# Kernel optimization log

Measured on AMD Instinct MI355X. Metric: run time of the kernel, lower is better.

Reference implementation:

```python
import jax, jax.numpy as jnp
import numpy as np

B, L, D = 16384, 5, 1024  # batch, lesionNum, feat_dim == att_dim
LN_EPS = 1e-5


def _layernorm(x, g, b):
    mu = jnp.mean(x, axis=-1, keepdims=True)
    var = jnp.var(x, axis=-1, keepdims=True)
    return (x - mu) * jax.lax.rsqrt(var + LN_EPS) * g + b


def setup_inputs() -> dict:
    key = jax.random.key(0)
    ks = jax.random.split(key, 8)
    s = 0.02
    x = jax.random.normal(ks[0], (B, L, D), dtype=jnp.float32)
    mask = jax.random.randint(ks[1], (1, L), 0, 2, dtype=jnp.int64)
    mask = mask.at[0, 0].set(1)  # guarantee at least one unmasked position
    Wq = jax.random.normal(ks[2], (D, D), dtype=jnp.float32) * s
    Wk = jax.random.normal(ks[3], (D, D), dtype=jnp.float32) * s
    Wv = jax.random.normal(ks[4], (D, D), dtype=jnp.float32) * s
    W1 = jax.random.normal(ks[5], (D, D), dtype=jnp.float32) * s
    b1 = jnp.zeros((D,), dtype=jnp.float32)
    W2 = jax.random.normal(ks[6], (D, D), dtype=jnp.float32) * s
    b2 = jnp.zeros((D,), dtype=jnp.float32)
    att_g = jnp.ones((D,), dtype=jnp.float32)
    att_b = jnp.zeros((D,), dtype=jnp.float32)
    ff_g = jnp.ones((D,), dtype=jnp.float32)
    ff_b = jnp.zeros((D,), dtype=jnp.float32)
    return dict(x=x, mask=mask, Wq=Wq, Wk=Wk, Wv=Wv, W1=W1, b1=b1, W2=W2,
                b2=b2, att_g=att_g, att_b=att_b, ff_g=ff_g, ff_b=ff_b)


def reference(x, mask, Wq, Wk, Wv, W1, b1, W2, b2, att_g, att_b, ff_g, ff_b):
    # QKV (no bias). With nhead=1 the reshape makes scores per-token dot
    # products: (B,L,1,D) @ (B,L,D,1) -> (B,L,1,1); we keep them as (B,L).
    q = jnp.einsum('bld,ed->ble', x, Wq)
    k = jnp.einsum('bld,ed->ble', x, Wk)
    v = jnp.einsum('bld,ed->ble', x, Wv)
    scores = jnp.sum(q * k, axis=-1) / jnp.sqrt(jnp.float32(D))  # (B,L)
    # torch loop sets -inf where ANY mask row has 0 (applied to all batches)
    keep = jnp.all(mask != 0, axis=0)  # (L,)
    scores = jnp.where(keep[None, :], scores, -jnp.inf)
    probs = jax.nn.softmax(scores, axis=1)  # softmax over token dim (dim=1)
    probs = jnp.where(jnp.isnan(probs), 0.0, probs)  # nan-safe (all-masked)
    attn = probs[:, :, None] * v  # (B,L,1,1)@(B,L,1,D) == per-token scaling
    y = _layernorm(attn + x, att_g, att_b)
    # FFN: Linear -> exact GELU -> Linear (dropout inactive in eval)
    h = jax.nn.gelu(jnp.einsum('bld,ed->ble', y, W1) + b1, approximate=False)
    ff = jnp.einsum('bld,ed->ble', h, W2) + b2
    return _layernorm(ff + y, ff_g, ff_b)
```

## Files before the change

### kernel.cpp

```cpp
#include <hip/hip_runtime.h>
#include <hip/hip_bf16.h>
#include <cstdint>


typedef float f32x4 __attribute__((ext_vector_type(4)));
typedef __bf16 bf16x8 __attribute__((ext_vector_type(8)));

#define DD 1024
#define NROWS 81920L

__device__ __forceinline__ unsigned short f2bf(float f) {
  union { float f; unsigned u; } c; c.f = f;
  unsigned u = c.u;
  return (unsigned short)((u + 0x7FFFu + ((u >> 16) & 1u)) >> 16);
}
__device__ __forceinline__ float bf2f(unsigned short b) {
  union { unsigned u; float f; } c; c.u = ((unsigned)b) << 16;
  return c.f;
}
__device__ __forceinline__ void unpack8(uint4 v, float* o) {
  o[0] = bf2f((unsigned short)(v.x & 0xffffu)); o[1] = bf2f((unsigned short)(v.x >> 16));
  o[2] = bf2f((unsigned short)(v.y & 0xffffu)); o[3] = bf2f((unsigned short)(v.y >> 16));
  o[4] = bf2f((unsigned short)(v.z & 0xffffu)); o[5] = bf2f((unsigned short)(v.z >> 16));
  o[6] = bf2f((unsigned short)(v.w & 0xffffu)); o[7] = bf2f((unsigned short)(v.w >> 16));
}
__device__ __forceinline__ void gload_lds16(const void* g, void* l) {
  __builtin_amdgcn_global_load_lds(
      (const __attribute__((address_space(1))) unsigned int*)g,
      (__attribute__((address_space(3))) unsigned int*)l, 16, 0, 0);
}

__global__ void __launch_bounds__(256) k_cvt_bf16(const float* __restrict__ in,
                                                  unsigned short* __restrict__ out, long n) {
  long i = ((long)blockIdx.x * blockDim.x + threadIdx.x) * 8;
  long stride = (long)gridDim.x * blockDim.x * 8;
  for (; i < n; i += stride) {
    f32x4 a = *(const f32x4*)(in + i);
    f32x4 b = *(const f32x4*)(in + i + 4);
    uint4 o;
    o.x = (unsigned)f2bf(a[0]) | ((unsigned)f2bf(a[1]) << 16);
    o.y = (unsigned)f2bf(a[2]) | ((unsigned)f2bf(a[3]) << 16);
    o.z = (unsigned)f2bf(b[0]) | ((unsigned)f2bf(b[1]) << 16);
    o.w = (unsigned)f2bf(b[2]) | ((unsigned)f2bf(b[3]) << 16);
    *(uint4*)(out + i) = o;
  }
}

__global__ void __launch_bounds__(256) k_gt(const float* __restrict__ Wq,
                                            const float* __restrict__ Wk,
                                            unsigned short* __restrict__ Gt) {
  __shared__ float sk[16][16];
  __shared__ float sq[16][64];
  const int tx = threadIdx.x, ty = threadIdx.y;
  const int n0 = blockIdx.y * 16;
  const int k0 = blockIdx.x * 64;
  float acc[4] = {0.f, 0.f, 0.f, 0.f};
  for (int e0 = 0; e0 < 1024; e0 += 16) {
    sk[ty][tx] = Wk[(long)(e0 + ty) * DD + n0 + tx];
    *(f32x4*)&sq[ty][tx * 4] = *(const f32x4*)&Wq[(long)(e0 + ty) * DD + k0 + tx * 4];
    __syncthreads();
#pragma unroll
    for (int ee = 0; ee < 16; ++ee) {
      float kv = sk[ee][ty];
      f32x4 qv = *(const f32x4*)&sq[ee][tx * 4];
      acc[0] += kv * qv[0]; acc[1] += kv * qv[1];
      acc[2] += kv * qv[2]; acc[3] += kv * qv[3];
    }
    __syncthreads();
  }
  uint2 o;
  o.x = (unsigned)f2bf(acc[0]) | ((unsigned)f2bf(acc[1]) << 16);
  o.y = (unsigned)f2bf(acc[2]) | ((unsigned)f2bf(acc[3]) << 16);
  *(uint2*)&Gt[(long)(n0 + ty) * DD + k0 + tx * 4] = o;
}


#define TILE(T, RSLOT, SSLOT, CA, CB, NA, NB, DOREAD, DOSTAGE, VM4)            \
  {                                                                            \
    if (VM4) { asm volatile("s_waitcnt vmcnt(4)" ::: "memory"); }              \
    else     { asm volatile("s_waitcnt vmcnt(0)" ::: "memory"); }              \
    __builtin_amdgcn_s_barrier();                                              \
    asm volatile("" ::: "memory");                                             \
    if (DOREAD) {                                                              \
      const char* bn_ = ldsB + (RSLOT) * 32768;                                \
      _Pragma("unroll") for (int mi = 0; mi < 8; ++mi)                         \
        NA[mi] = *(const bf16x8*)(bn_ + aoff[mi]);                             \
      _Pragma("unroll") for (int nj = 0; nj < 4; ++nj)                         \
        NB[nj] = *(const bf16x8*)(bn_ + 16384 + boff[nj]);                     \
    }                                                                          \
    if (DOSTAGE) stage((T) + 3, ldsB + (SSLOT) * 32768);                       \
    __builtin_amdgcn_sched_barrier(0);                                         \
    __builtin_amdgcn_s_setprio(1);                                             \
    _Pragma("unroll") for (int mi = 0; mi < 8; ++mi)                           \
      _Pragma("unroll") for (int nj = 0; nj < 4; ++nj)                         \
        acc[mi][nj] = __builtin_amdgcn_mfma_f32_16x16x32_bf16(                 \
            CA[mi], CB[nj], acc[mi][nj], 0, 0, 0);                             \
    __builtin_amdgcn_s_setprio(0);                                             \
  }

template <int EPI>
__global__ void __launch_bounds__(512, 2) k_gemm256(
    const unsigned short* __restrict__ A,
    const unsigned short* __restrict__ B,
    unsigned short* __restrict__ outb,
    float* __restrict__ outf,
    const float* __restrict__ bias,
    const unsigned short* __restrict__ resid,
    const int ntl2,
    const int cst) {
  __shared__ __align__(16) char ldsB[131072];
  const int tid = threadIdx.x;
  const int lane = tid & 63;
  const int wid = tid >> 6;
  const int wm = wid >> 2, wn = wid & 3;

  const int nwg = gridDim.x;
  const int cpx = nwg >> 3;
  const int dd = blockIdx.x;
  const int lgc = (dd & 7) * cpx + (dd >> 3);
  const int mt = lgc >> ntl2;
  const int nt = lgc & ((1 << ntl2) - 1);
  const long m0 = (long)mt * 256;
  const int n0 = nt * 256;

  const int srow = tid >> 2;
  const int oc = ((tid & 3) << 4) ^ (((srow >> 1) & 3) << 4);
  const char* gA0 = (const char*)A + (m0 + srow) * 2048 + oc;
  const char* gA1 = gA0 + 128 * 2048;
  const char* gB0 = (const char*)B + ((long)n0 + srow) * 2048 + oc;
  const char* gB1 = gB0 + 128 * 2048;
  const int d0 = tid * 16;

  auto stage = [&](int kt, char* base) {
    const long ko = (long)kt << 6;
    gload_lds16(gA0 + ko, base + d0);
    gload_lds16(gA1 + ko, base + 8192 + d0);
    gload_lds16(gB0 + ko, base + 16384 + d0);
    gload_lds16(gB1 + ko, base + 24576 + d0);
  };

  const int la = lane & 15, lg = lane >> 4;
  const int cb = ((lg ^ ((la >> 1) & 3)) << 4);
  int aoff[8], boff[4];
#pragma unroll
  for (int mi = 0; mi < 8; ++mi) aoff[mi] = (wm * 128 + mi * 16 + la) * 64 + cb;
#pragma unroll
  for (int nj = 0; nj < 4; ++nj) boff[nj] = (wn * 64 + nj * 16 + la) * 64 + cb;

  f32x4 acc[8][4];
#pragma unroll
  for (int mi = 0; mi < 8; ++mi)
#pragma unroll
    for (int nj = 0; nj < 4; ++nj) acc[mi][nj] = f32x4{0.f, 0.f, 0.f, 0.f};

  stage(0, ldsB);
  stage(1, ldsB + 32768);
  stage(2, ldsB + 65536);
  asm volatile("s_waitcnt vmcnt(8)" ::: "memory");
  __builtin_amdgcn_s_barrier();
  asm volatile("" ::: "memory");

  bf16x8 a0[8], b0[4], a1[8], b1[4];
#pragma unroll
  for (int mi = 0; mi < 8; ++mi) a0[mi] = *(const bf16x8*)(ldsB + aoff[mi]);
#pragma unroll
  for (int nj = 0; nj < 4; ++nj) b0[nj] = *(const bf16x8*)(ldsB + 16384 + boff[nj]);

  for (int t0 = 0; t0 < 28; t0 += 4) {
    TILE(t0 + 0, 1, 3, a0, b0, a1, b1, true, true, true);
    TILE(t0 + 1, 2, 0, a1, b1, a0, b0, true, true, true);
    TILE(t0 + 2, 3, 1, a0, b0, a1, b1, true, true, true);
    TILE(t0 + 3, 0, 2, a1, b1, a0, b0, true, true, true);
  }
  TILE(28, 1, 3, a0, b0, a1, b1, true, true, true);
  TILE(29, 2, 0, a1, b1, a0, b0, true, false, true);
  TILE(30, 3, 1, a0, b0, a1, b1, true, false, false);
  TILE(31, 0, 2, a1, b1, a0, b0, false, false, false);

  const long rbase = m0 + wm * 128 + (lane >> 4) * 4;
  const int cbase = n0 + wn * 64 + la;
#pragma unroll
  for (int mi = 0; mi < 8; ++mi) {
#pragma unroll
    for (int nj = 0; nj < 4; ++nj) {
      const int col = cbase + nj * 16;
      float bv = 0.f;
      if constexpr (EPI != 0) bv = bias[col];
#pragma unroll
      for (int t = 0; t < 4; ++t) {
        const long r = rbase + mi * 16 + t;
        float v = acc[mi][nj][t];
        if constexpr (EPI == 0) {
          outb[r * (long)cst + col] = f2bf(v);
        } else if constexpr (EPI == 1) {
          v += bv;
          v = 0.5f * v * (1.0f + erff(v * 0.70710678118654752f));
          outb[r * (long)cst + col] = f2bf(v);
        } else if constexpr (EPI == 2) {
          v += bv + bf2f(resid[r * (long)cst + col]);
          outf[r * (long)cst + col] = v;
        } else {
          v += bv + bf2f(resid[r * (long)cst + col]);
          outb[r * (long)cst + col] = f2bf(v);
        }
      }
    }
  }
}

__global__ void __launch_bounds__(256) k_attn_ln(
    const unsigned short* __restrict__ xb, const unsigned short* __restrict__ uv,
    unsigned short* __restrict__ yb, const int* __restrict__ mask,
    const float* __restrict__ att_g, const float* __restrict__ att_b) {
  const int b = blockIdx.x * 4 + (threadIdx.x >> 6);
  const int lane = threadIdx.x & 63;
  const long xbase = (long)b * 5120 + lane * 16;
  const long ubase = (long)b * 10240 + lane * 16;

  float xr[5][16];
  float sc[5];
#pragma unroll
  for (int l = 0; l < 5; ++l) {
    const unsigned short* xp = xb + xbase + l * 1024;
    const unsigned short* up = uv + ubase + l * 2048;
    unpack8(*(const uint4*)xp, xr[l]); unpack8(*(const uint4*)(xp + 8), xr[l] + 8);
    float uu[16];
    unpack8(*(const uint4*)up, uu); unpack8(*(const uint4*)(up + 8), uu + 8);
    float d = 0.f;
#pragma unroll
    for (int c = 0; c < 16; ++c) d += xr[l][c] * uu[c];
#pragma unroll
    for (int off = 32; off; off >>= 1) d += __shfl_xor(d, off);
    sc[l] = d * 0.03125f;
  }
  bool keep[5];
  float m = -1e30f;
#pragma unroll
  for (int l = 0; l < 5; ++l) {
    keep[l] = (mask[l] != 0);
    if (keep[l]) m = fmaxf(m, sc[l]);
  }
  float p[5], s = 0.f;
#pragma unroll
  for (int l = 0; l < 5; ++l) {
    p[l] = keep[l] ? __expf(sc[l] - m) : 0.f;
    s += p[l];
  }
  const float inv = 1.f / s;

  float gg[16], bb[16];
  {
    const float* gp = att_g + lane * 16;
    const float* bp = att_b + lane * 16;
#pragma unroll
    for (int q = 0; q < 4; ++q) {
      f32x4 gv = *(const f32x4*)(gp + q * 4);
      f32x4 bv = *(const f32x4*)(bp + q * 4);
#pragma unroll
      for (int c = 0; c < 4; ++c) { gg[q * 4 + c] = gv[c]; bb[q * 4 + c] = bv[c]; }
    }
  }

#pragma unroll
  for (int l = 0; l < 5; ++l) {
    const unsigned short* vp = uv + ubase + l * 2048 + 1024;
    float vv[16];
    unpack8(*(const uint4*)vp, vv); unpack8(*(const uint4*)(vp + 8), vv + 8);
    const float pl = p[l] * inv;
    float t[16], sm = 0.f, sq = 0.f;
#pragma unroll
    for (int c = 0; c < 16; ++c) {
      t[c] = pl * vv[c] + xr[l][c];
      sm += t[c];
      sq += t[c] * t[c];
    }
#pragma unroll
    for (int off = 32; off; off >>= 1) {
      sm += __shfl_xor(sm, off);
      sq += __shfl_xor(sq, off);
    }
    const float mu = sm * (1.f / 1024.f);
    const float var = sq * (1.f / 1024.f) - mu * mu;
    const float rs = rsqrtf(var + 1e-5f);
    unsigned short r[16];
#pragma unroll
    for (int c = 0; c < 16; ++c) r[c] = f2bf((t[c] - mu) * rs * gg[c] + bb[c]);
    uint4 o0, o1;
    o0.x = (unsigned)r[0] | ((unsigned)r[1] << 16);  o0.y = (unsigned)r[2] | ((unsigned)r[3] << 16);
    o0.z = (unsigned)r[4] | ((unsigned)r[5] << 16);  o0.w = (unsigned)r[6] | ((unsigned)r[7] << 16);
    o1.x = (unsigned)r[8] | ((unsigned)r[9] << 16);  o1.y = (unsigned)r[10] | ((unsigned)r[11] << 16);
    o1.z = (unsigned)r[12] | ((unsigned)r[13] << 16); o1.w = (unsigned)r[14] | ((unsigned)r[15] << 16);
    unsigned short* yp = yb + xbase + l * 1024;
    *(uint4*)yp = o0;
    *(uint4*)(yp + 8) = o1;
  }
}

__global__ void __launch_bounds__(256) k_ln_final_bf(const unsigned short* __restrict__ zb,
                                                     float* __restrict__ out,
                                                     const float* __restrict__ g,
                                                     const float* __restrict__ bb) {
  const int lane = threadIdx.x & 63;
  const long row = (long)blockIdx.x * 4 + (threadIdx.x >> 6);
  const unsigned short* p = zb + row * DD + lane * 16;
  float t[16];
  unpack8(*(const uint4*)p, t);
  unpack8(*(const uint4*)(p + 8), t + 8);
  float sm = 0.f, sq = 0.f;
#pragma unroll
  for (int c = 0; c < 16; ++c) { sm += t[c]; sq += t[c] * t[c]; }
#pragma unroll
  for (int off = 32; off; off >>= 1) {
    sm += __shfl_xor(sm, off);
    sq += __shfl_xor(sq, off);
  }
  const float mu = sm * (1.f / 1024.f);
  const float var = sq * (1.f / 1024.f) - mu * mu;
  const float rs = rsqrtf(var + 1e-5f);
  float* op = out + row * DD + lane * 16;
  const float* gp = g + lane * 16;
  const float* bp = bb + lane * 16;
#pragma unroll
  for (int q = 0; q < 4; ++q) {
    f32x4 gv = *(const f32x4*)(gp + q * 4);
    f32x4 bv = *(const f32x4*)(bp + q * 4);
    f32x4 o;
#pragma unroll
    for (int c = 0; c < 4; ++c) o[c] = (t[q * 4 + c] - mu) * rs * gv[c] + bv[c];
    *(f32x4*)(op + q * 4) = o;
  }
}

__global__ void __launch_bounds__(256) k_ln_final(float* __restrict__ z,
                                                  const float* __restrict__ g,
                                                  const float* __restrict__ bb) {
  const int lane = threadIdx.x & 63;
  const long row = (long)blockIdx.x * 4 + (threadIdx.x >> 6);
  float* p = z + row * DD + lane * 16;
  f32x4 v[4];
  float sm = 0.f, sq = 0.f;
#pragma unroll
  for (int q = 0; q < 4; ++q) {
    v[q] = *(const f32x4*)(p + q * 4);
#pragma unroll
    for (int c = 0; c < 4; ++c) { sm += v[q][c]; sq += v[q][c] * v[q][c]; }
  }
#pragma unroll
  for (int off = 32; off; off >>= 1) {
    sm += __shfl_xor(sm, off);
    sq += __shfl_xor(sq, off);
  }
  const float mu = sm * (1.f / 1024.f);
  const float var = sq * (1.f / 1024.f) - mu * mu;
  const float rs = rsqrtf(var + 1e-5f);
  const float* gp = g + lane * 16;
  const float* bp = bb + lane * 16;
#pragma unroll
  for (int q = 0; q < 4; ++q) {
    f32x4 gv = *(const f32x4*)(gp + q * 4);
    f32x4 bv = *(const f32x4*)(bp + q * 4);
#pragma unroll
    for (int c = 0; c < 4; ++c) v[q][c] = (v[q][c] - mu) * rs * gv[c] + bv[c];
    *(f32x4*)(p + q * 4) = v[q];
  }
}

extern "C" void kernel_launch(void* const* d_in, const int* in_sizes, int n_in,
                              void* d_out, int out_size, void* d_ws, size_t ws_size,
                              hipStream_t stream) {
  const float* x     = (const float*)d_in[0];
  const int*   mask  = (const int*)d_in[1];
  const float* Wq    = (const float*)d_in[2];
  const float* Wk    = (const float*)d_in[3];
  const float* Wv    = (const float*)d_in[4];
  const float* W1    = (const float*)d_in[5];
  const float* b1    = (const float*)d_in[6];
  const float* W2    = (const float*)d_in[7];
  const float* b2    = (const float*)d_in[8];
  const float* att_g = (const float*)d_in[9];
  const float* att_b = (const float*)d_in[10];
  const float* ff_g  = (const float*)d_in[11];
  const float* ff_b  = (const float*)d_in[12];

  const long NE = NROWS * DD;
  unsigned short* xb   = (unsigned short*)d_ws;
  unsigned short* hb   = xb + NE;
  unsigned short* Bcat = hb + NE;
  unsigned short* W1b  = Bcat + 2L * DD * DD;
  unsigned short* W2b  = W1b + (long)DD * DD;
  unsigned short* zb   = W2b + (long)DD * DD;

  const size_t need_zb = (size_t)(3L * NE + 4L * DD * DD) * 2;
  const bool use_zb = ws_size >= need_zb;

  unsigned short* uvb = (unsigned short*)d_out;
  float* outf = (float*)d_out;

  k_cvt_bf16<<<2048, 256, 0, stream>>>(x, xb, NE);
  k_cvt_bf16<<<512, 256, 0, stream>>>(Wv, Bcat + (long)DD * DD, (long)DD * DD);
  k_cvt_bf16<<<512, 256, 0, stream>>>(W1, W1b, (long)DD * DD);
  k_cvt_bf16<<<512, 256, 0, stream>>>(W2, W2b, (long)DD * DD);
  k_gt<<<dim3(16, 64), dim3(16, 16), 0, stream>>>(Wq, Wk, Bcat);

  k_gemm256<0><<<2560, 512, 0, stream>>>(xb, Bcat, uvb, nullptr, nullptr, nullptr, 3, 2048);
  k_attn_ln<<<4096, 256, 0, stream>>>(xb, uvb, xb, mask, att_g, att_b);
  k_gemm256<1><<<1280, 512, 0, stream>>>(xb, W1b, hb, nullptr, b1, nullptr, 2, 1024);
  if (use_zb) {
    k_gemm256<3><<<1280, 512, 0, stream>>>(hb, W2b, zb, nullptr, b2, xb, 2, 1024);
    k_ln_final_bf<<<20480, 256, 0, stream>>>(zb, outf, ff_g, ff_b);
  } else {
    k_gemm256<2><<<1280, 512, 0, stream>>>(hb, W2b, nullptr, outf, b2, xb, 2, 1024);
    k_ln_final<<<20480, 256, 0, stream>>>(outf, ff_g, ff_b);
  }
}
```

Measured before the change: 1.287 ms.

## Restructure GEMM main loop into 8-phase ping-pong schedule with split fragment loads

Replaces the 4-slot, register-double-buffered K loop with a two-buffer ping-pong over K=128 super-steps, each split into four phases. Every phase loads half of the A fragments plus the B fragments from LDS, issues one stage of the next super-step's A or B, and runs 16 MFMAs, with barriers between phases. The aim is lower register pressure, since only one fragment set is held instead of two, and finer interleaving of LDS reads, global-to-LDS copies and MFMA work. In exchange it adds more barriers per K step and waits on lgkmcnt(0) before each MFMA group, which exposes LDS read latency.

Result: faster. 1.247 ms (-3.1%).

```diff
diff --git a/kernel.cpp b/kernel.cpp
--- a/kernel.cpp
+++ b/kernel.cpp
@@ -75,27 +75,34 @@
 }
 
 
-#define TILE(T, RSLOT, SSLOT, CA, CB, NA, NB, DOREAD, DOSTAGE, VM4)            \
+#define PHASE(BUFC, KK, MIH, DOSTAGE, STG_ISB, STG_KK, SN, TRAILV)             \
   {                                                                            \
-    if (VM4) { asm volatile("s_waitcnt vmcnt(4)" ::: "memory"); }              \
-    else     { asm volatile("s_waitcnt vmcnt(0)" ::: "memory"); }              \
+    const char* rb_ = (BUFC) + ((KK) << 14);                                   \
+    if ((MIH) == 0) {                                                          \
+      _Pragma("unroll") for (int j = 0; j < 4; ++j)                            \
+        fb[j] = *(const bf16x8*)(rb_ + boff[j]);                               \
+      _Pragma("unroll") for (int i = 0; i < 4; ++i)                            \
+        fa[i] = *(const bf16x8*)(rb_ + aoff[i]);                               \
+    } else {                                                                   \
+      _Pragma("unroll") for (int i = 0; i < 4; ++i)                            \
+        fa[i] = *(const bf16x8*)(rb_ + aoff[4 + i]);                           \
+    }                                                                          \
+    if (DOSTAGE) {                                                             \
+      if (STG_ISB) stageB((SN), (STG_KK)); else stageA((SN), (STG_KK));        \
+    }                                                                          \
+    __builtin_amdgcn_s_barrier();                                              \
+    asm volatile("s_waitcnt lgkmcnt(0)" ::: "memory");                         \
+    __builtin_amdgcn_sched_barrier(0);                                         \
+    __builtin_amdgcn_s_setprio(1);                                             \
+    _Pragma("unroll") for (int i = 0; i < 4; ++i)                              \
+      _Pragma("unroll") for (int j = 0; j < 4; ++j)                            \
+        acc[(MIH) * 4 + i][j] = __builtin_amdgcn_mfma_f32_16x16x32_bf16(       \
+            fa[i], fb[j], acc[(MIH) * 4 + i][j], 0, 0, 0);                     \
+    __builtin_amdgcn_s_setprio(0);                                             \
+    if ((TRAILV) == 1) asm volatile("s_waitcnt vmcnt(4)" ::: "memory");        \
+    else if ((TRAILV) == 2) asm volatile("s_waitcnt vmcnt(0)" ::: "memory");   \
     __builtin_amdgcn_s_barrier();                                              \
     asm volatile("" ::: "memory");                                             \
-    if (DOREAD) {                                                              \
-      const char* bn_ = ldsB + (RSLOT) * 32768;                                \
-      _Pragma("unroll") for (int mi = 0; mi < 8; ++mi)                         \
-        NA[mi] = *(const bf16x8*)(bn_ + aoff[mi]);                             \
-      _Pragma("unroll") for (int nj = 0; nj < 4; ++nj)                         \
-        NB[nj] = *(const bf16x8*)(bn_ + 16384 + boff[nj]);                     \
-    }                                                                          \
-    if (DOSTAGE) stage((T) + 3, ldsB + (SSLOT) * 32768);                       \
-    __builtin_amdgcn_sched_barrier(0);                                         \
-    __builtin_amdgcn_s_setprio(1);                                             \
-    _Pragma("unroll") for (int mi = 0; mi < 8; ++mi)                           \
-      _Pragma("unroll") for (int nj = 0; nj < 4; ++nj)                         \
-        acc[mi][nj] = __builtin_amdgcn_mfma_f32_16x16x32_bf16(                 \
-            CA[mi], CB[nj], acc[mi][nj], 0, 0, 0);                             \
-    __builtin_amdgcn_s_setprio(0);                                             \
   }
 
 template <int EPI>
@@ -123,20 +130,23 @@
   const long m0 = (long)mt * 256;
   const int n0 = nt * 256;
 
-  const int srow = tid >> 2;
-  const int oc = ((tid & 3) << 4) ^ (((srow >> 1) & 3) << 4);
-  const char* gA0 = (const char*)A + (m0 + srow) * 2048 + oc;
-  const char* gA1 = gA0 + 128 * 2048;
-  const char* gB0 = (const char*)B + ((long)n0 + srow) * 2048 + oc;
-  const char* gB1 = gB0 + 128 * 2048;
-  const int d0 = tid * 16;
-
-  auto stage = [&](int kt, char* base) {
-    const long ko = (long)kt << 6;
-    gload_lds16(gA0 + ko, base + d0);
-    gload_lds16(gA1 + ko, base + 8192 + d0);
-    gload_lds16(gB0 + ko, base + 16384 + d0);
-    gload_lds16(gB1 + ko, base + 24576 + d0);
+  const int q = tid >> 2;
+  const int gcol = (((tid & 3) ^ ((q >> 1) & 3)) << 4);
+  const char* gA = (const char*)A + (m0 + q) * 2048 + gcol;
+  const char* gB = (const char*)B + ((long)n0 + q) * 2048 + gcol;
+  const int ldst = tid * 16;
+
+  auto stageA = [&](int s, int kk) {
+    char* dst = ldsB + ((s & 1) << 16) + (kk << 14) + ldst;
+    const char* src = gA + (long)s * 128 + (kk << 6);
+    gload_lds16(src, dst);
+    gload_lds16(src + 128 * 2048, dst + 8192);
+  };
+  auto stageB = [&](int s, int kk) {
+    char* dst = ldsB + ((s & 1) << 16) + 32768 + (kk << 14) + ldst;
+    const char* src = gB + (long)s * 128 + (kk << 6);
+    gload_lds16(src, dst);
+    gload_lds16(src + 128 * 2048, dst + 8192);
   };
 
   const int la = lane & 15, lg = lane >> 4;
@@ -145,7 +155,7 @@
 #pragma unroll
   for (int mi = 0; mi < 8; ++mi) aoff[mi] = (wm * 128 + mi * 16 + la) * 64 + cb;
 #pragma unroll
-  for (int nj = 0; nj < 4; ++nj) boff[nj] = (wn * 64 + nj * 16 + la) * 64 + cb;
+  for (int nj = 0; nj < 4; ++nj) boff[nj] = 32768 + (wn * 64 + nj * 16 + la) * 64 + cb;
 
   f32x4 acc[8][4];
 #pragma unroll
@@ -153,29 +163,28 @@
 #pragma unroll
     for (int nj = 0; nj < 4; ++nj) acc[mi][nj] = f32x4{0.f, 0.f, 0.f, 0.f};
 
-  stage(0, ldsB);
-  stage(1, ldsB + 32768);
-  stage(2, ldsB + 65536);
-  asm volatile("s_waitcnt vmcnt(8)" ::: "memory");
+  bf16x8 fa[4], fb[4];
+
+  stageA(0, 0); stageB(0, 0); stageA(0, 1); stageB(0, 1);
+  asm volatile("s_waitcnt vmcnt(4)" ::: "memory");
   __builtin_amdgcn_s_barrier();
   asm volatile("" ::: "memory");
 
-  bf16x8 a0[8], b0[4], a1[8], b1[4];
-#pragma unroll
-  for (int mi = 0; mi < 8; ++mi) a0[mi] = *(const bf16x8*)(ldsB + aoff[mi]);
-#pragma unroll
-  for (int nj = 0; nj < 4; ++nj) b0[nj] = *(const bf16x8*)(ldsB + 16384 + boff[nj]);
-
-  for (int t0 = 0; t0 < 28; t0 += 4) {
-    TILE(t0 + 0, 1, 3, a0, b0, a1, b1, true, true, true);
-    TILE(t0 + 1, 2, 0, a1, b1, a0, b0, true, true, true);
-    TILE(t0 + 2, 3, 1, a0, b0, a1, b1, true, true, true);
-    TILE(t0 + 3, 0, 2, a1, b1, a0, b0, true, true, true);
-  }
-  TILE(28, 1, 3, a0, b0, a1, b1, true, true, true);
-  TILE(29, 2, 0, a1, b1, a0, b0, true, false, true);
-  TILE(30, 3, 1, a0, b0, a1, b1, true, false, false);
-  TILE(31, 0, 2, a1, b1, a0, b0, false, false, false);
+  for (int s = 0; s < 15; ++s) {
+    const int sn = s + 1;
+    char* bufc = ldsB + ((s & 1) << 16);
+    PHASE(bufc, 0, 0, true, false, 0, sn, 0);
+    PHASE(bufc, 0, 1, true, true,  0, sn, 1);
+    PHASE(bufc, 1, 0, true, false, 1, sn, 0);
+    PHASE(bufc, 1, 1, true, true,  1, sn, 1);
+  }
+  {
+    char* bufc = ldsB + ((15 & 1) << 16);
+    PHASE(bufc, 0, 0, false, false, 0, 16, 0);
+    PHASE(bufc, 0, 1, false, false, 0, 16, 2);
+    PHASE(bufc, 1, 0, false, false, 1, 16, 0);
+    PHASE(bufc, 1, 1, false, false, 1, 16, 0);
+  }
 
   const long rbase = m0 + wm * 128 + (lane >> 4) * 4;
   const int cbase = n0 + wn * 64 + la;
```

## Fuse score dot-product into QKV GEMM epilogue and shorten LDS pipeline to three stages

Applied to the files above, without the earlier changes.

The first GEMM's epilogue now computes each row's partial score x·(G x) for its column tiles directly and writes 16 float partials per row. The u half of the output is no longer stored in bf16 and re-read; only v is written. The attention kernel then sums these partials instead of reloading u and computing dot products. Separately, the main GEMM loop changes from a 4-buffer prefetch-depth-3 schedule with register double-buffered fragments to a 3-buffer depth-2 schedule with the barrier after compute. This cuts LDS use, but LDS loads may now be less hidden.

New measurement: 1.271 ms. No clear change (-1.3%).

```diff
diff --git a/kernel.cpp b/kernel.cpp
--- a/kernel.cpp
+++ b/kernel.cpp
@@ -75,27 +75,28 @@
 }
 
 
-#define TILE(T, RSLOT, SSLOT, CA, CB, NA, NB, DOREAD, DOSTAGE, VM4)            \
+#define STEP(RBUF, SBUF, S, DOSTAGE, TAILV)                                    \
   {                                                                            \
-    if (VM4) { asm volatile("s_waitcnt vmcnt(4)" ::: "memory"); }              \
-    else     { asm volatile("s_waitcnt vmcnt(0)" ::: "memory"); }              \
-    __builtin_amdgcn_s_barrier();                                              \
-    asm volatile("" ::: "memory");                                             \
-    if (DOREAD) {                                                              \
-      const char* bn_ = ldsB + (RSLOT) * 32768;                                \
-      _Pragma("unroll") for (int mi = 0; mi < 8; ++mi)                         \
-        NA[mi] = *(const bf16x8*)(bn_ + aoff[mi]);                             \
-      _Pragma("unroll") for (int nj = 0; nj < 4; ++nj)                         \
-        NB[nj] = *(const bf16x8*)(bn_ + 16384 + boff[nj]);                     \
+    const char* bA_ = ldsB + (RBUF) * 32768;                                   \
+    const char* bB_ = bA_ + 16384;                                             \
+    bf16x8 fa[8], fb[4];                                                       \
+    _Pragma("unroll") for (int i = 0; i < 8; ++i)                              \
+      fa[i] = *(const bf16x8*)(bA_ + aoff[i]);                                 \
+    _Pragma("unroll") for (int j = 0; j < 4; ++j)                              \
+      fb[j] = *(const bf16x8*)(bB_ + boff[j]);                                 \
+    if (DOSTAGE) stage((S) + 2, ldsB + (SBUF) * 32768);                        \
+    __builtin_amdgcn_s_setprio(1);                                             \
+    _Pragma("unroll") for (int i = 0; i < 8; ++i)                              \
+      _Pragma("unroll") for (int j = 0; j < 4; ++j)                            \
+        acc[i][j] = __builtin_amdgcn_mfma_f32_16x16x32_bf16(                   \
+            fa[i], fb[j], acc[i][j], 0, 0, 0);                                 \
+    __builtin_amdgcn_s_setprio(0);                                             \
+    if ((TAILV) == 1) asm volatile("s_waitcnt vmcnt(4)" ::: "memory");         \
+    else if ((TAILV) == 2) asm volatile("s_waitcnt vmcnt(0)" ::: "memory");    \
+    if ((TAILV) != 3) {                                                        \
+      __builtin_amdgcn_s_barrier();                                            \
+      asm volatile("" ::: "memory");                                           \
     }                                                                          \
-    if (DOSTAGE) stage((T) + 3, ldsB + (SSLOT) * 32768);                       \
-    __builtin_amdgcn_sched_barrier(0);                                         \
-    __builtin_amdgcn_s_setprio(1);                                             \
-    _Pragma("unroll") for (int mi = 0; mi < 8; ++mi)                           \
-      _Pragma("unroll") for (int nj = 0; nj < 4; ++nj)                         \
-        acc[mi][nj] = __builtin_amdgcn_mfma_f32_16x16x32_bf16(                 \
-            CA[mi], CB[nj], acc[mi][nj], 0, 0, 0);                             \
-    __builtin_amdgcn_s_setprio(0);                                             \
   }
 
 template <int EPI>
@@ -106,9 +107,10 @@
     float* __restrict__ outf,
     const float* __restrict__ bias,
     const unsigned short* __restrict__ resid,
+    float* __restrict__ scp,
     const int ntl2,
     const int cst) {
-  __shared__ __align__(16) char ldsB[131072];
+  __shared__ __align__(16) char ldsB[98304];
   const int tid = threadIdx.x;
   const int lane = tid & 63;
   const int wid = tid >> 6;
@@ -123,20 +125,19 @@
   const long m0 = (long)mt * 256;
   const int n0 = nt * 256;
 
-  const int srow = tid >> 2;
-  const int oc = ((tid & 3) << 4) ^ (((srow >> 1) & 3) << 4);
-  const char* gA0 = (const char*)A + (m0 + srow) * 2048 + oc;
-  const char* gA1 = gA0 + 128 * 2048;
-  const char* gB0 = (const char*)B + ((long)n0 + srow) * 2048 + oc;
-  const char* gB1 = gB0 + 128 * 2048;
-  const int d0 = tid * 16;
-
-  auto stage = [&](int kt, char* base) {
-    const long ko = (long)kt << 6;
-    gload_lds16(gA0 + ko, base + d0);
-    gload_lds16(gA1 + ko, base + 8192 + d0);
-    gload_lds16(gB0 + ko, base + 16384 + d0);
-    gload_lds16(gB1 + ko, base + 24576 + d0);
+  const int q = tid >> 2;
+  const int gcol = (((tid & 3) ^ ((q >> 1) & 3)) << 4);
+  const char* gA = (const char*)A + (m0 + q) * 2048 + gcol;
+  const char* gB = (const char*)B + ((long)n0 + q) * 2048 + gcol;
+  const int ldst = tid * 16;
+
+  auto stage = [&](int s, char* base) {
+    const char* sa = gA + (long)s * 64;
+    const char* sb = gB + (long)s * 64;
+    gload_lds16(sa, base + ldst);
+    gload_lds16(sa + 128 * 2048, base + 8192 + ldst);
+    gload_lds16(sb, base + 16384 + ldst);
+    gload_lds16(sb + 128 * 2048, base + 24576 + ldst);
   };
 
   const int la = lane & 15, lg = lane >> 4;
@@ -155,83 +156,97 @@
 
   stage(0, ldsB);
   stage(1, ldsB + 32768);
-  stage(2, ldsB + 65536);
-  asm volatile("s_waitcnt vmcnt(8)" ::: "memory");
+  asm volatile("s_waitcnt vmcnt(4)" ::: "memory");
   __builtin_amdgcn_s_barrier();
   asm volatile("" ::: "memory");
 
-  bf16x8 a0[8], b0[4], a1[8], b1[4];
-#pragma unroll
-  for (int mi = 0; mi < 8; ++mi) a0[mi] = *(const bf16x8*)(ldsB + aoff[mi]);
-#pragma unroll
-  for (int nj = 0; nj < 4; ++nj) b0[nj] = *(const bf16x8*)(ldsB + 16384 + boff[nj]);
-
-  for (int t0 = 0; t0 < 28; t0 += 4) {
-    TILE(t0 + 0, 1, 3, a0, b0, a1, b1, true, true, true);
-    TILE(t0 + 1, 2, 0, a1, b1, a0, b0, true, true, true);
-    TILE(t0 + 2, 3, 1, a0, b0, a1, b1, true, true, true);
-    TILE(t0 + 3, 0, 2, a1, b1, a0, b0, true, true, true);
-  }
-  TILE(28, 1, 3, a0, b0, a1, b1, true, true, true);
-  TILE(29, 2, 0, a1, b1, a0, b0, true, false, true);
-  TILE(30, 3, 1, a0, b0, a1, b1, true, false, false);
-  TILE(31, 0, 2, a1, b1, a0, b0, false, false, false);
+  for (int st = 0; st < 30; st += 3) {
+    STEP(0, 2, st + 0, true, 1);
+    STEP(1, 0, st + 1, true, 1);
+    STEP(2, 1, st + 2, true, 1);
+  }
+  STEP(0, 2, 30, false, 2);
+  STEP(1, 0, 31, false, 3);
 
   const long rbase = m0 + wm * 128 + (lane >> 4) * 4;
   const int cbase = n0 + wn * 64 + la;
-#pragma unroll
-  for (int mi = 0; mi < 8; ++mi) {
-#pragma unroll
-    for (int nj = 0; nj < 4; ++nj) {
-      const int col = cbase + nj * 16;
-      float bv = 0.f;
-      if constexpr (EPI != 0) bv = bias[col];
-#pragma unroll
-      for (int t = 0; t < 4; ++t) {
-        const long r = rbase + mi * 16 + t;
-        float v = acc[mi][nj][t];
-        if constexpr (EPI == 0) {
-          outb[r * (long)cst + col] = f2bf(v);
-        } else if constexpr (EPI == 1) {
-          v += bv;
-          v = 0.5f * v * (1.0f + erff(v * 0.70710678118654752f));
-          outb[r * (long)cst + col] = f2bf(v);
-        } else if constexpr (EPI == 2) {
-          v += bv + bf2f(resid[r * (long)cst + col]);
-          outf[r * (long)cst + col] = v;
-        } else {
-          v += bv + bf2f(resid[r * (long)cst + col]);
-          outb[r * (long)cst + col] = f2bf(v);
+  if constexpr (EPI == 0) {
+    if (n0 < 1024) {
+      float* sp = scp + ((long)(n0 >> 8) * 4 + wn) * NROWS;
+#pragma unroll
+      for (int mi = 0; mi < 8; ++mi) {
+#pragma unroll
+        for (int t = 0; t < 4; ++t) {
+          const long r = rbase + mi * 16 + t;
+          float s = 0.f;
+#pragma unroll
+          for (int nj = 0; nj < 4; ++nj)
+            s += acc[mi][nj][t] * bf2f(A[r * DD + cbase + nj * 16]);
+          s += __shfl_xor(s, 1);
+          s += __shfl_xor(s, 2);
+          s += __shfl_xor(s, 4);
+          s += __shfl_xor(s, 8);
+          if (la == 0) sp[r] = s;
         }
       }
+    } else {
+#pragma unroll
+      for (int mi = 0; mi < 8; ++mi)
+#pragma unroll
+        for (int nj = 0; nj < 4; ++nj) {
+          const int col = cbase + nj * 16 - 1024;
+#pragma unroll
+          for (int t = 0; t < 4; ++t) {
+            const long r = rbase + mi * 16 + t;
+            outb[r * 1024 + col] = f2bf(acc[mi][nj][t]);
+          }
+        }
+    }
+  } else {
+#pragma unroll
+    for (int mi = 0; mi < 8; ++mi) {
+#pragma unroll
+      for (int nj = 0; nj < 4; ++nj) {
+        const int col = cbase + nj * 16;
+        const float bv = bias[col];
+#pragma unroll
+        for (int t = 0; t < 4; ++t) {
+          const long r = rbase + mi * 16 + t;
+          float v = acc[mi][nj][t];
+          if constexpr (EPI == 1) {
+            v += bv;
+            v = 0.5f * v * (1.0f + erff(v * 0.70710678118654752f));
+            outb[r * (long)cst + col] = f2bf(v);
+          } else if constexpr (EPI == 2) {
+            v += bv + bf2f(resid[r * (long)cst + col]);
+            outf[r * (long)cst + col] = v;
+          } else {
+            v += bv + bf2f(resid[r * (long)cst + col]);
+            outb[r * (long)cst + col] = f2bf(v);
+          }
+        }
+      }
     }
   }
 }
 
 __global__ void __launch_bounds__(256) k_attn_ln(
-    const unsigned short* __restrict__ xb, const unsigned short* __restrict__ uv,
-    unsigned short* __restrict__ yb, const int* __restrict__ mask,
-    const float* __restrict__ att_g, const float* __restrict__ att_b) {
+    const unsigned short* __restrict__ xb, const unsigned short* __restrict__ vb,
+    unsigned short* __restrict__ yb, const float* __restrict__ scp,
+    const int* __restrict__ mask, const float* __restrict__ att_g,
+    const float* __restrict__ att_b) {
   const int b = blockIdx.x * 4 + (threadIdx.x >> 6);
   const int lane = threadIdx.x & 63;
-  const long xbase = (long)b * 5120 + lane * 16;
-  const long ubase = (long)b * 10240 + lane * 16;
-
-  float xr[5][16];
+  const long base = (long)b * 5120 + lane * 16;
+
   float sc[5];
 #pragma unroll
   for (int l = 0; l < 5; ++l) {
-    const unsigned short* xp = xb + xbase + l * 1024;
-    const unsigned short* up = uv + ubase + l * 2048;
-    unpack8(*(const uint4*)xp, xr[l]); unpack8(*(const uint4*)(xp + 8), xr[l] + 8);
-    float uu[16];
-    unpack8(*(const uint4*)up, uu); unpack8(*(const uint4*)(up + 8), uu + 8);
-    float d = 0.f;
-#pragma unroll
-    for (int c = 0; c < 16; ++c) d += xr[l][c] * uu[c];
-#pragma unroll
-    for (int off = 32; off; off >>= 1) d += __shfl_xor(d, off);
-    sc[l] = d * 0.03125f;
+    const long r = (long)b * 5 + l;
+    float s = 0.f;
+#pragma unroll
+    for (int k = 0; k < 16; ++k) s += scp[(long)k * NROWS + r];
+    sc[l] = s * 0.03125f;
   }
   bool keep[5];
   float m = -1e30f;
@@ -263,14 +278,16 @@
 
 #pragma unroll
   for (int l = 0; l < 5; ++l) {
-    const unsigned short* vp = uv + ubase + l * 2048 + 1024;
-    float vv[16];
+    const unsigned short* xp = xb + base + l * 1024;
+    const unsigned short* vp = vb + base + l * 1024;
+    float xr[16], vv[16];
+    unpack8(*(const uint4*)xp, xr); unpack8(*(const uint4*)(xp + 8), xr + 8);
     unpack8(*(const uint4*)vp, vv); unpack8(*(const uint4*)(vp + 8), vv + 8);
     const float pl = p[l] * inv;
     float t[16], sm = 0.f, sq = 0.f;
 #pragma unroll
     for (int c = 0; c < 16; ++c) {
-      t[c] = pl * vv[c] + xr[l][c];
+      t[c] = pl * vv[c] + xr[c];
       sm += t[c];
       sq += t[c] * t[c];
     }
@@ -290,7 +307,7 @@
     o0.z = (unsigned)r[4] | ((unsigned)r[5] << 16);  o0.w = (unsigned)r[6] | ((unsigned)r[7] << 16);
     o1.x = (unsigned)r[8] | ((unsigned)r[9] << 16);  o1.y = (unsigned)r[10] | ((unsigned)r[11] << 16);
     o1.z = (unsigned)r[12] | ((unsigned)r[13] << 16); o1.w = (unsigned)r[14] | ((unsigned)r[15] << 16);
-    unsigned short* yp = yb + xbase + l * 1024;
+    unsigned short* yp = yb + base + l * 1024;
     *(uint4*)yp = o0;
     *(uint4*)(yp + 8) = o1;
   }
@@ -388,12 +405,13 @@
   unsigned short* Bcat = hb + NE;
   unsigned short* W1b  = Bcat + 2L * DD * DD;
   unsigned short* W2b  = W1b + (long)DD * DD;
-  unsigned short* zb   = W2b + (long)DD * DD;
-
-  const size_t need_zb = (size_t)(3L * NE + 4L * DD * DD) * 2;
+  float*          scp  = (float*)(W2b + (long)DD * DD);
+  unsigned short* zb   = (unsigned short*)(scp + 16 * NROWS);
+
+  const size_t need_zb = (size_t)(3L * NE + 4L * DD * DD) * 2 + 16 * NROWS * 4;
   const bool use_zb = ws_size >= need_zb;
 
-  unsigned short* uvb = (unsigned short*)d_out;
+  unsigned short* vb = (unsigned short*)d_out;
   float* outf = (float*)d_out;
 
   k_cvt_bf16<<<2048, 256, 0, stream>>>(x, xb, NE);
@@ -402,14 +420,14 @@
   k_cvt_bf16<<<512, 256, 0, stream>>>(W2, W2b, (long)DD * DD);
   k_gt<<<dim3(16, 64), dim3(16, 16), 0, stream>>>(Wq, Wk, Bcat);
 
-  k_gemm256<0><<<2560, 512, 0, stream>>>(xb, Bcat, uvb, nullptr, nullptr, nullptr, 3, 2048);
-  k_attn_ln<<<4096, 256, 0, stream>>>(xb, uvb, xb, mask, att_g, att_b);
-  k_gemm256<1><<<1280, 512, 0, stream>>>(xb, W1b, hb, nullptr, b1, nullptr, 2, 1024);
+  k_gemm256<0><<<2560, 512, 0, stream>>>(xb, Bcat, vb, nullptr, nullptr, nullptr, scp, 3, 1024);
+  k_attn_ln<<<4096, 256, 0, stream>>>(xb, vb, xb, scp, mask, att_g, att_b);
+  k_gemm256<1><<<1280, 512, 0, stream>>>(xb, W1b, hb, nullptr, b1, nullptr, nullptr, 2, 1024);
   if (use_zb) {
-    k_gemm256<3><<<1280, 512, 0, stream>>>(hb, W2b, zb, nullptr, b2, xb, 2, 1024);
+    k_gemm256<3><<<1280, 512, 0, stream>>>(hb, W2b, zb, nullptr, b2, xb, nullptr, 2, 1024);
     k_ln_final_bf<<<20480, 256, 0, stream>>>(zb, outf, ff_g, ff_b);
   } else {
-    k_gemm256<2><<<1280, 512, 0, stream>>>(hb, W2b, nullptr, outf, b2, xb, 2, 1024);
+    k_gemm256<2><<<1280, 512, 0, stream>>>(hb, W2b, nullptr, outf, b2, xb, nullptr, 2, 1024);
     k_ln_final<<<20480, 256, 0, stream>>>(outf, ff_g, ff_b);
   }
 }
```
